# Kernel tuning notes

Measured on AMD Instinct MI355X. Metric: run time of the kernel, lower is better.

The kernel has to match this reference:

```python
import jax, jax.numpy as jnp
from jax import lax
import numpy as np

B, T, I, H, O = 256, 512, 64, 512, 16


def setup_inputs() -> dict:
    key = jax.random.key(0)
    ks = jax.random.split(key, 8)
    s = 1.0 / np.sqrt(H)  # torch RNN/Linear init scale
    return {
        "x": jax.random.normal(ks[0], (B, T, I), dtype=jnp.float32),
        "h0": jnp.zeros((1, B, H), dtype=jnp.float32),
        "W_ih": jax.random.uniform(ks[1], (H, I), jnp.float32, -s, s),
        "W_hh": jax.random.uniform(ks[2], (H, H), jnp.float32, -s, s),
        "b_ih": jax.random.uniform(ks[3], (H,), jnp.float32, -s, s),
        "b_hh": jax.random.uniform(ks[4], (H,), jnp.float32, -s, s),
        "W_fc": jax.random.uniform(ks[5], (O, H), jnp.float32, -s, s),
        "b_fc": jax.random.uniform(ks[6], (O,), jnp.float32, -s, s),
    }


def reference(x, h0, W_ih, W_hh, b_ih, b_hh, W_fc, b_fc):
    # Precompute input projection for all timesteps: (B,T,H)
    xp = jnp.einsum("bti,hi->bth", x, W_ih) + b_ih + b_hh
    W_hh_T = W_hh.T

    def step(h, xt):  # h: (B,H), xt: (B,H)
        h_new = jax.nn.relu(xt + h @ W_hh_T)
        return h_new, None

    h_last, _ = lax.scan(step, h0[0], jnp.swapaxes(xp, 0, 1))  # (B,H)
    out = h_last @ W_fc.T + b_fc  # (B,O)
    # torch module returns (out.unsqueeze(2), hidden) with hidden=(layers,B,H)
    return out[:, :, None], h_last[None, :, :]
```

## Files before the change

kernel.cpp:

```cpp
#include <hip/hip_runtime.h>

#define B_ 256
#define T_ 512
#define I_ 64
#define H_ 512
#define O_ 16

typedef _Float16 half8 __attribute__((ext_vector_type(8)));
typedef _Float16 half4 __attribute__((ext_vector_type(4)));
typedef float    f32x4 __attribute__((ext_vector_type(4)));

#define MFMA16(a, b, c) __builtin_amdgcn_mfma_f32_16x16x32_f16((a), (b), (c), 0, 0, 0)

__device__ inline half8 cvt_h8(f32x4 a, f32x4 b) {
  half8 v;
  v[0] = (_Float16)a[0]; v[1] = (_Float16)a[1]; v[2] = (_Float16)a[2]; v[3] = (_Float16)a[3];
  v[4] = (_Float16)b[0]; v[5] = (_Float16)b[1]; v[6] = (_Float16)b[2]; v[7] = (_Float16)b[3];
  return v;
}

__global__ __launch_bounds__(256, 2)
void xp_prepass(const float* __restrict__ x, const float* __restrict__ W_ih,
                const float* __restrict__ b_ih, const float* __restrict__ b_hh,
                _Float16* __restrict__ xp) {
  const int tid = threadIdx.x, L = tid & 63, w = tid >> 6;
  const int n = L & 15, kq = (L >> 4) & 3;
  const int g = blockIdx.x & 15, tc = blockIdx.x >> 4;

  __shared__ __attribute__((aligned(16))) _Float16 wlih[32 * 2 * 64 * 8];
  __shared__ float biasl[512];
  const half8* wlih8 = (const half8*)wlih;

  #pragma unroll
  for (int u = 0; u < 16; ++u) {
    const int s = tid + u * 256;
    const int jt = s >> 7, c = (s >> 6) & 1, Lp = s & 63;
    const int jl = Lp & 15, kq2 = Lp >> 4;
    const float* p = W_ih + (jt * 16 + jl) * I_ + c * 32 + kq2 * 8;
    ((half8*)wlih)[s] = cvt_h8(*(const f32x4*)(p), *(const f32x4*)(p + 4));
  }
  #pragma unroll
  for (int u = 0; u < 2; ++u) {
    const int idx = tid + u * 256;
    biasl[idx] = b_ih[idx] + b_hh[idx];
  }
  __syncthreads();

  half8 xb[4][2];
  #pragma unroll
  for (int rr = 0; rr < 4; ++rr) {
    const int t = tc * 16 + w * 4 + rr;
    const float* p = x + ((size_t)(g * 16 + n) * T_ + t) * I_ + kq * 8;
    xb[rr][0] = cvt_h8(*(const f32x4*)(p),      *(const f32x4*)(p + 4));
    xb[rr][1] = cvt_h8(*(const f32x4*)(p + 32), *(const f32x4*)(p + 36));
  }

  #pragma unroll 1
  for (int hi = 0; hi < 8; ++hi) {
    half8 o[4][2];
    #pragma unroll
    for (int jt2 = 0; jt2 < 4; ++jt2) {
      const int jt = hi * 4 + jt2;
      const half8 a0 = wlih8[(jt * 2 + 0) * 64 + L];
      const half8 a1 = wlih8[(jt * 2 + 1) * 64 + L];
      const f32x4 bv = *(const f32x4*)&biasl[jt * 16 + 4 * kq];
      #pragma unroll
      for (int rr = 0; rr < 4; ++rr) {
        f32x4 acc; acc[0] = 0.f; acc[1] = 0.f; acc[2] = 0.f; acc[3] = 0.f;
        acc = MFMA16(a0, xb[rr][0], acc);
        acc = MFMA16(a1, xb[rr][1], acc);
        #pragma unroll
        for (int i = 0; i < 4; ++i)
          o[rr][jt2 >> 1][(jt2 & 1) * 4 + i] = (_Float16)(acc[i] + bv[i]);
      }
    }
    #pragma unroll
    for (int rr = 0; rr < 4; ++rr) {
      const int t = tc * 16 + w * 4 + rr;
      _Float16* dst = xp + ((size_t)(t * 16 + g) * 512 + hi * 64 + L) * 16;
      *(half8*)(dst)     = o[rr][0];
      *(half8*)(dst + 8) = o[rr][1];
    }
  }
}

__global__ __launch_bounds__(512, 2)
void rnn_persist(const float* __restrict__ h0, const float* __restrict__ W_hh,
                 const float* __restrict__ W_fc, const float* __restrict__ b_fc,
                 float* __restrict__ out, const _Float16* __restrict__ xp) {
  const int tid = threadIdx.x;
  const int L   = tid & 63;
  const int w   = tid >> 6;
  const int n   = L & 15;
  const int kq  = (L >> 4) & 3;
  const int g   = blockIdx.x;

  __shared__ __attribute__((aligned(16))) _Float16 hb[2 * 16 * 64 * 8];
  __shared__ __attribute__((aligned(16))) _Float16 wlds[8 * 12 * 64 * 8];
  half8* hb8 = (half8*)hb;
  const half8* wl8 = (const half8*)wlds;
  half8* wlw = (half8*)wlds;

  half8 whA[32];
  half8 whV[20];
  #pragma unroll
  for (int ln = 0; ln < 4; ++ln) {
    const int j = w * 64 + ln * 16 + n;
    #pragma unroll
    for (int kc = 0; kc < 8; ++kc) {
      const f32x4* p = (const f32x4*)(W_hh + j * H_ + kc * 32 + kq * 8);
      whA[ln * 8 + kc] = cvt_h8(p[0], p[1]);
    }
    #pragma unroll
    for (int kc = 0; kc < 5; ++kc) {
      const f32x4* p = (const f32x4*)(W_hh + j * H_ + (8 + kc) * 32 + kq * 8);
      whV[ln * 5 + kc] = cvt_h8(p[0], p[1]);
    }
    #pragma unroll
    for (int s = 0; s < 3; ++s) {
      const f32x4* p = (const f32x4*)(W_hh + j * H_ + (13 + s) * 32 + kq * 8);
      wlw[(w * 12 + s * 4 + ln) * 64 + L] = cvt_h8(p[0], p[1]);
    }
  }
  #pragma unroll
  for (int i2 = 0; i2 < 32; ++i2) asm volatile("" : "+a"(whA[i2]));

  #pragma unroll
  for (int u = 0; u < 2; ++u) {
    const int S = tid + u * 512;
    const int k8 = S >> 4, nb = S & 15;
    const float* p = h0 + (g * 16 + nb) * H_ + k8 * 8;
    hb8[S] = cvt_h8(*(const f32x4*)(p), *(const f32x4*)(p + 4));
  }
  __syncthreads();

  half8 xq0, xq1;
  {
    const half8* p0 = (const half8*)(xp + ((size_t)(0 * 16 + g) * 512 + tid) * 16);
    xq0 = p0[0]; xq1 = p0[1];
  }

  #pragma unroll 1
  for (int t = 0; t < T_; ++t) {
    const half8* hbr = hb8 + (t & 1) * 1024;
    half8* hbw = hb8 + ((t + 1) & 1) * 1024;

    f32x4 acc[4];
    #pragma unroll
    for (int ln = 0; ln < 4; ++ln)
      #pragma unroll
      for (int i = 0; i < 4; ++i)
        acc[ln][i] = (float)((ln < 2 ? xq0 : xq1)[(ln & 1) * 4 + i]);

    {
      const int tn = (t + 1) & (T_ - 1);
      const half8* pn = (const half8*)(xp + ((size_t)(tn * 16 + g) * 512 + tid) * 16);
      xq0 = pn[0]; xq1 = pn[1];
    }

    #pragma unroll
    for (int kc = 0; kc < 8; ++kc) {
      const half8 b = hbr[kc * 64 + L];
      #pragma unroll
      for (int ln = 0; ln < 4; ++ln) acc[ln] = MFMA16(whA[ln * 8 + kc], b, acc[ln]);
    }
    #pragma unroll
    for (int kc = 0; kc < 5; ++kc) {
      const half8 b = hbr[(8 + kc) * 64 + L];
      #pragma unroll
      for (int ln = 0; ln < 4; ++ln) acc[ln] = MFMA16(whV[ln * 5 + kc], b, acc[ln]);
    }
    #pragma unroll
    for (int s = 0; s < 3; ++s) {
      const half8 b = hbr[(13 + s) * 64 + L];
      #pragma unroll
      for (int ln = 0; ln < 4; ++ln)
        acc[ln] = MFMA16(wl8[(w * 12 + s * 4 + ln) * 64 + L], b, acc[ln]);
    }

    #pragma unroll
    for (int ln = 0; ln < 4; ++ln) {
      half4 hv;
      #pragma unroll
      for (int i = 0; i < 4; ++i) hv[i] = (_Float16)fmaxf(acc[ln][i], 0.f);
      const int S = (w * 8 + ln * 2 + (kq >> 1)) * 16 + n;
      *(half4*)((_Float16*)hbw + S * 8 + 4 * (kq & 1)) = hv;
    }
    __syncthreads();
  }

  const half8* hf = hb8;
  #pragma unroll
  for (int u = 0; u < 2; ++u) {
    const int ri = tid + u * 512;
    const int k8 = ri >> 4, nb = ri & 15;
    const half8 v = hf[k8 * 16 + nb];
    float* dst = out + 4096 + (g * 16 + nb) * H_ + k8 * 8;
    #pragma unroll
    for (int e = 0; e < 8; ++e) dst[e] = (float)v[e];
  }
  __syncthreads();
  float* wfcf = (float*)wlds;
  #pragma unroll
  for (int u = 0; u < 16; ++u) {
    const int idx = tid + u * 512;
    wfcf[(idx >> 9) * 513 + (idx & 511)] = W_fc[idx];
  }
  __syncthreads();
  if (tid < 256) {
    const int bl = tid >> 4, o = tid & 15;
    float s = 0.f;
    #pragma unroll 8
    for (int k8 = 0; k8 < 64; ++k8) {
      const half8 v = hf[k8 * 16 + bl];
      #pragma unroll
      for (int e = 0; e < 8; ++e) s += (float)v[e] * wfcf[o * 513 + k8 * 8 + e];
    }
    out[(g * 16 + bl) * 16 + o] = s + b_fc[o];
  }
}

extern "C" void kernel_launch(void* const* d_in, const int* in_sizes, int n_in,
                              void* d_out, int out_size, void* d_ws, size_t ws_size,
                              hipStream_t stream) {
  const float* x    = (const float*)d_in[0];
  const float* h0   = (const float*)d_in[1];
  const float* W_ih = (const float*)d_in[2];
  const float* W_hh = (const float*)d_in[3];
  const float* b_ih = (const float*)d_in[4];
  const float* b_hh = (const float*)d_in[5];
  const float* W_fc = (const float*)d_in[6];
  const float* b_fc = (const float*)d_in[7];
  float* out = (float*)d_out;

  _Float16* xp = (_Float16*)d_ws;

  xp_prepass<<<dim3(512), dim3(256), 0, stream>>>(x, W_ih, b_ih, b_hh, xp);
  rnn_persist<<<dim3(16), dim3(512), 0, stream>>>(h0, W_hh, W_fc, b_fc, out, xp);
}
```

Measured before the change: 892.0 us.

## Rotate per-wave K order and prefetch own h chunk before barrier

Each wave now walks the K chunks of the recurrent matmul starting at its own freshly written chunk (2*W), rotating the weight register assignment to match. This lets it read its first B operand right after its own stores and before the barrier, so the first MFMAs of the next step can start with no LDS wait. The per-wave rotation also spreads LDS reads across different addresses. The price is eight template instantiations behind a switch, which increases code size. The final h is still left in buffer 0 because T is even.

```diff
diff --git a/kernel.cpp b/kernel.cpp
--- a/kernel.cpp
+++ b/kernel.cpp
@@ -84,6 +84,104 @@
   }
 }
 
+template <int W>
+__device__ __forceinline__ void rnn_core(const float* __restrict__ W_hh,
+                                         const _Float16* __restrict__ xp,
+                                         half8* hb8, half8* wl8w,
+                                         const int g, const int L) {
+  const int n  = L & 15;
+  const int kq = (L >> 4) & 3;
+  const int tid = W * 64 + L;
+
+  half8 whA[32];
+  half8 whV[20];
+  #pragma unroll
+  for (int ln = 0; ln < 4; ++ln) {
+    const int j = W * 64 + ln * 16 + n;
+    #pragma unroll
+    for (int p = 0; p < 8; ++p) {
+      const int kc = (2 * W + p) & 15;
+      const f32x4* s = (const f32x4*)(W_hh + j * H_ + kc * 32 + kq * 8);
+      whA[ln * 8 + p] = cvt_h8(s[0], s[1]);
+    }
+    #pragma unroll
+    for (int p = 8; p < 13; ++p) {
+      const int kc = (2 * W + p) & 15;
+      const f32x4* s = (const f32x4*)(W_hh + j * H_ + kc * 32 + kq * 8);
+      whV[ln * 5 + (p - 8)] = cvt_h8(s[0], s[1]);
+    }
+    #pragma unroll
+    for (int p = 13; p < 16; ++p) {
+      const int kc = (2 * W + p) & 15;
+      const f32x4* s = (const f32x4*)(W_hh + j * H_ + kc * 32 + kq * 8);
+      wl8w[((p - 13) * 4 + ln) * 64 + L] = cvt_h8(s[0], s[1]);
+    }
+  }
+  #pragma unroll
+  for (int i2 = 0; i2 < 32; ++i2) asm volatile("" : "+a"(whA[i2]));
+
+  half8 xq0, xq1;
+  {
+    const half8* p0 = (const half8*)(xp + ((size_t)(0 * 16 + g) * 512 + tid) * 16);
+    xq0 = p0[0]; xq1 = p0[1];
+  }
+
+  half8* rb = hb8;
+  half8* wb = hb8 + 1024;
+  half8 bq0 = rb[((2 * W) & 15) * 64 + L];
+
+  #pragma unroll 1
+  for (int t = 0; t < T_; ++t) {
+    f32x4 acc[4];
+    #pragma unroll
+    for (int ln = 0; ln < 4; ++ln)
+      #pragma unroll
+      for (int i = 0; i < 4; ++i)
+        acc[ln][i] = (float)((ln < 2 ? xq0 : xq1)[(ln & 1) * 4 + i]);
+
+    {
+      const int tn = (t + 1) & (T_ - 1);
+      const half8* pn = (const half8*)(xp + ((size_t)(tn * 16 + g) * 512 + tid) * 16);
+      xq0 = pn[0]; xq1 = pn[1];
+    }
+
+    #pragma unroll
+    for (int ln = 0; ln < 4; ++ln) acc[ln] = MFMA16(whA[ln * 8 + 0], bq0, acc[ln]);
+    #pragma unroll
+    for (int p = 1; p < 8; ++p) {
+      const half8 b = rb[((2 * W + p) & 15) * 64 + L];
+      #pragma unroll
+      for (int ln = 0; ln < 4; ++ln) acc[ln] = MFMA16(whA[ln * 8 + p], b, acc[ln]);
+    }
+    #pragma unroll
+    for (int p = 8; p < 13; ++p) {
+      const half8 b = rb[((2 * W + p) & 15) * 64 + L];
+      #pragma unroll
+      for (int ln = 0; ln < 4; ++ln) acc[ln] = MFMA16(whV[ln * 5 + (p - 8)], b, acc[ln]);
+    }
+    #pragma unroll
+    for (int p = 13; p < 16; ++p) {
+      const half8 b = rb[((2 * W + p) & 15) * 64 + L];
+      #pragma unroll
+      for (int ln = 0; ln < 4; ++ln)
+        acc[ln] = MFMA16(wl8w[((p - 13) * 4 + ln) * 64 + L], b, acc[ln]);
+    }
+
+    #pragma unroll
+    for (int ln = 0; ln < 4; ++ln) {
+      half4 hv;
+      #pragma unroll
+      for (int i = 0; i < 4; ++i) hv[i] = (_Float16)fmaxf(acc[ln][i], 0.f);
+      const int S = (W * 8 + ln * 2 + (kq >> 1)) * 16 + n;
+      *(half4*)((_Float16*)wb + S * 8 + 4 * (kq & 1)) = hv;
+    }
+    bq0 = wb[((2 * W) & 15) * 64 + L];
+
+    __syncthreads();
+    half8* tmp = rb; rb = wb; wb = tmp;
+  }
+}
+
 __global__ __launch_bounds__(512, 2)
 void rnn_persist(const float* __restrict__ h0, const float* __restrict__ W_hh,
                  const float* __restrict__ W_fc, const float* __restrict__ b_fc,
@@ -91,39 +189,11 @@
   const int tid = threadIdx.x;
   const int L   = tid & 63;
   const int w   = tid >> 6;
-  const int n   = L & 15;
-  const int kq  = (L >> 4) & 3;
   const int g   = blockIdx.x;
 
   __shared__ __attribute__((aligned(16))) _Float16 hb[2 * 16 * 64 * 8];
   __shared__ __attribute__((aligned(16))) _Float16 wlds[8 * 12 * 64 * 8];
   half8* hb8 = (half8*)hb;
-  const half8* wl8 = (const half8*)wlds;
-  half8* wlw = (half8*)wlds;
-
-  half8 whA[32];
-  half8 whV[20];
-  #pragma unroll
-  for (int ln = 0; ln < 4; ++ln) {
-    const int j = w * 64 + ln * 16 + n;
-    #pragma unroll
-    for (int kc = 0; kc < 8; ++kc) {
-      const f32x4* p = (const f32x4*)(W_hh + j * H_ + kc * 32 + kq * 8);
-      whA[ln * 8 + kc] = cvt_h8(p[0], p[1]);
-    }
-    #pragma unroll
-    for (int kc = 0; kc < 5; ++kc) {
-      const f32x4* p = (const f32x4*)(W_hh + j * H_ + (8 + kc) * 32 + kq * 8);
-      whV[ln * 5 + kc] = cvt_h8(p[0], p[1]);
-    }
-    #pragma unroll
-    for (int s = 0; s < 3; ++s) {
-      const f32x4* p = (const f32x4*)(W_hh + j * H_ + (13 + s) * 32 + kq * 8);
-      wlw[(w * 12 + s * 4 + ln) * 64 + L] = cvt_h8(p[0], p[1]);
-    }
-  }
-  #pragma unroll
-  for (int i2 = 0; i2 < 32; ++i2) asm volatile("" : "+a"(whA[i2]));
 
   #pragma unroll
   for (int u = 0; u < 2; ++u) {
@@ -134,59 +204,17 @@
   }
   __syncthreads();
 
-  half8 xq0, xq1;
-  {
-    const half8* p0 = (const half8*)(xp + ((size_t)(0 * 16 + g) * 512 + tid) * 16);
-    xq0 = p0[0]; xq1 = p0[1];
-  }
-
-  #pragma unroll 1
-  for (int t = 0; t < T_; ++t) {
-    const half8* hbr = hb8 + (t & 1) * 1024;
-    half8* hbw = hb8 + ((t + 1) & 1) * 1024;
-
-    f32x4 acc[4];
-    #pragma unroll
-    for (int ln = 0; ln < 4; ++ln)
-      #pragma unroll
-      for (int i = 0; i < 4; ++i)
-        acc[ln][i] = (float)((ln < 2 ? xq0 : xq1)[(ln & 1) * 4 + i]);
-
-    {
-      const int tn = (t + 1) & (T_ - 1);
-      const half8* pn = (const half8*)(xp + ((size_t)(tn * 16 + g) * 512 + tid) * 16);
-      xq0 = pn[0]; xq1 = pn[1];
-    }
-
-    #pragma unroll
-    for (int kc = 0; kc < 8; ++kc) {
-      const half8 b = hbr[kc * 64 + L];
-      #pragma unroll
-      for (int ln = 0; ln < 4; ++ln) acc[ln] = MFMA16(whA[ln * 8 + kc], b, acc[ln]);
-    }
-    #pragma unroll
-    for (int kc = 0; kc < 5; ++kc) {
-      const half8 b = hbr[(8 + kc) * 64 + L];
-      #pragma unroll
-      for (int ln = 0; ln < 4; ++ln) acc[ln] = MFMA16(whV[ln * 5 + kc], b, acc[ln]);
-    }
-    #pragma unroll
-    for (int s = 0; s < 3; ++s) {
-      const half8 b = hbr[(13 + s) * 64 + L];
-      #pragma unroll
-      for (int ln = 0; ln < 4; ++ln)
-        acc[ln] = MFMA16(wl8[(w * 12 + s * 4 + ln) * 64 + L], b, acc[ln]);
-    }
-
-    #pragma unroll
-    for (int ln = 0; ln < 4; ++ln) {
-      half4 hv;
-      #pragma unroll
-      for (int i = 0; i < 4; ++i) hv[i] = (_Float16)fmaxf(acc[ln][i], 0.f);
-      const int S = (w * 8 + ln * 2 + (kq >> 1)) * 16 + n;
-      *(half4*)((_Float16*)hbw + S * 8 + 4 * (kq & 1)) = hv;
-    }
-    __syncthreads();
+  half8* wl8w = (half8*)wlds + (w * 12) * 64;
+
+  switch (w) {
+    case 0: rnn_core<0>(W_hh, xp, hb8, wl8w, g, L); break;
+    case 1: rnn_core<1>(W_hh, xp, hb8, wl8w, g, L); break;
+    case 2: rnn_core<2>(W_hh, xp, hb8, wl8w, g, L); break;
+    case 3: rnn_core<3>(W_hh, xp, hb8, wl8w, g, L); break;
+    case 4: rnn_core<4>(W_hh, xp, hb8, wl8w, g, L); break;
+    case 5: rnn_core<5>(W_hh, xp, hb8, wl8w, g, L); break;
+    case 6: rnn_core<6>(W_hh, xp, hb8, wl8w, g, L); break;
+    default: rnn_core<7>(W_hh, xp, hb8, wl8w, g, L); break;
   }
 
   const half8* hf = hb8;
```

New measurement: 1.063 ms. 19.2% more time.

## Stream last four W_hh k-chunks from global/L2 each step instead of LDS

Applied to the files above, without the earlier changes.

Adds a staging kernel that writes the last four k-chunks of W_hh in fp16 MFMA-fragment layout to workspace. The recurrent kernel reloads these chunks from global memory (expected to be L2-resident) every timestep, double-buffering the loads across MFMA groups. This frees VGPRs, since whV shrinks from 20 to 12 registers, and cuts LDS weight reads to one chunk. The intent is to relieve register pressure and LDS-bandwidth contention in the serial loop, at the cost of per-step global-load latency on the critical path plus an extra kernel launch.

```diff
diff --git a/kernel.cpp b/kernel.cpp
--- a/kernel.cpp
+++ b/kernel.cpp
@@ -17,6 +17,22 @@
   v[0] = (_Float16)a[0]; v[1] = (_Float16)a[1]; v[2] = (_Float16)a[2]; v[3] = (_Float16)a[3];
   v[4] = (_Float16)b[0]; v[5] = (_Float16)b[1]; v[6] = (_Float16)b[2]; v[7] = (_Float16)b[3];
   return v;
+}
+
+__global__ __launch_bounds__(512, 1)
+void wstage(const float* __restrict__ W_hh, _Float16* __restrict__ wbuf) {
+  const int tid = threadIdx.x, L = tid & 63, w = tid >> 6;
+  const int n = L & 15, kq = (L >> 4) & 3;
+  half8* out8 = (half8*)wbuf;
+  #pragma unroll
+  for (int e = 0; e < 4; ++e)
+    #pragma unroll
+    for (int ln = 0; ln < 4; ++ln) {
+      const int j = w * 64 + ln * 16 + n;
+      const int kc = 12 + e;
+      const f32x4* s = (const f32x4*)(W_hh + j * H_ + kc * 32 + kq * 8);
+      out8[(w * 16 + e * 4 + ln) * 64 + L] = cvt_h8(s[0], s[1]);
+    }
 }
 
 __global__ __launch_bounds__(256, 2)
@@ -87,7 +103,8 @@
 __global__ __launch_bounds__(512, 2)
 void rnn_persist(const float* __restrict__ h0, const float* __restrict__ W_hh,
                  const float* __restrict__ W_fc, const float* __restrict__ b_fc,
-                 float* __restrict__ out, const _Float16* __restrict__ xp) {
+                 float* __restrict__ out, const _Float16* __restrict__ xp,
+                 const _Float16* __restrict__ wbuf) {
   const int tid = threadIdx.x;
   const int L   = tid & 63;
   const int w   = tid >> 6;
@@ -96,13 +113,13 @@
   const int g   = blockIdx.x;
 
   __shared__ __attribute__((aligned(16))) _Float16 hb[2 * 16 * 64 * 8];
-  __shared__ __attribute__((aligned(16))) _Float16 wlds[8 * 12 * 64 * 8];
+  __shared__ __attribute__((aligned(16))) char wsmem[16 * 513 * 4];
   half8* hb8 = (half8*)hb;
-  const half8* wl8 = (const half8*)wlds;
-  half8* wlw = (half8*)wlds;
+  half8* wlw = (half8*)wsmem;
+  const half8* wl8 = (const half8*)wsmem;
 
   half8 whA[32];
-  half8 whV[20];
+  half8 whV[12];
   #pragma unroll
   for (int ln = 0; ln < 4; ++ln) {
     const int j = w * 64 + ln * 16 + n;
@@ -112,14 +129,13 @@
       whA[ln * 8 + kc] = cvt_h8(p[0], p[1]);
     }
     #pragma unroll
-    for (int kc = 0; kc < 5; ++kc) {
-      const f32x4* p = (const f32x4*)(W_hh + j * H_ + (8 + kc) * 32 + kq * 8);
-      whV[ln * 5 + kc] = cvt_h8(p[0], p[1]);
-    }
-    #pragma unroll
-    for (int s = 0; s < 3; ++s) {
-      const f32x4* p = (const f32x4*)(W_hh + j * H_ + (13 + s) * 32 + kq * 8);
-      wlw[(w * 12 + s * 4 + ln) * 64 + L] = cvt_h8(p[0], p[1]);
+    for (int kc = 8; kc < 11; ++kc) {
+      const f32x4* p = (const f32x4*)(W_hh + j * H_ + kc * 32 + kq * 8);
+      whV[ln * 3 + (kc - 8)] = cvt_h8(p[0], p[1]);
+    }
+    {
+      const f32x4* p = (const f32x4*)(W_hh + j * H_ + 11 * 32 + kq * 8);
+      wlw[(w * 4 + ln) * 64 + L] = cvt_h8(p[0], p[1]);
     }
   }
   #pragma unroll
@@ -140,11 +156,23 @@
     xq0 = p0[0]; xq1 = p0[1];
   }
 
+  const half8* wsb_base = (const half8*)wbuf + (w * 16) * 64;
+  int zoff = 0;
+
   #pragma unroll 1
   for (int t = 0; t < T_; ++t) {
     const half8* hbr = hb8 + (t & 1) * 1024;
     half8* hbw = hb8 + ((t + 1) & 1) * 1024;
 
+    asm volatile("" : "+v"(zoff));
+    const half8* wsb = wsb_base + zoff;
+
+    half8 ws0[4], ws1[4];
+    #pragma unroll
+    for (int ln = 0; ln < 4; ++ln) ws0[ln] = wsb[(0 * 4 + ln) * 64 + L];
+    #pragma unroll
+    for (int ln = 0; ln < 4; ++ln) ws1[ln] = wsb[(1 * 4 + ln) * 64 + L];
+
     f32x4 acc[4];
     #pragma unroll
     for (int ln = 0; ln < 4; ++ln)
@@ -165,17 +193,40 @@
       for (int ln = 0; ln < 4; ++ln) acc[ln] = MFMA16(whA[ln * 8 + kc], b, acc[ln]);
     }
     #pragma unroll
-    for (int kc = 0; kc < 5; ++kc) {
-      const half8 b = hbr[(8 + kc) * 64 + L];
-      #pragma unroll
-      for (int ln = 0; ln < 4; ++ln) acc[ln] = MFMA16(whV[ln * 5 + kc], b, acc[ln]);
-    }
-    #pragma unroll
-    for (int s = 0; s < 3; ++s) {
-      const half8 b = hbr[(13 + s) * 64 + L];
+    for (int kc = 8; kc < 11; ++kc) {
+      const half8 b = hbr[kc * 64 + L];
+      #pragma unroll
+      for (int ln = 0; ln < 4; ++ln) acc[ln] = MFMA16(whV[ln * 3 + (kc - 8)], b, acc[ln]);
+    }
+    {
+      const half8 b = hbr[11 * 64 + L];
       #pragma unroll
       for (int ln = 0; ln < 4; ++ln)
-        acc[ln] = MFMA16(wl8[(w * 12 + s * 4 + ln) * 64 + L], b, acc[ln]);
+        acc[ln] = MFMA16(wl8[(w * 4 + ln) * 64 + L], b, acc[ln]);
+    }
+    {
+      const half8 b = hbr[12 * 64 + L];
+      #pragma unroll
+      for (int ln = 0; ln < 4; ++ln) acc[ln] = MFMA16(ws0[ln], b, acc[ln]);
+      #pragma unroll
+      for (int ln = 0; ln < 4; ++ln) ws0[ln] = wsb[(2 * 4 + ln) * 64 + L];
+    }
+    {
+      const half8 b = hbr[13 * 64 + L];
+      #pragma unroll
+      for (int ln = 0; ln < 4; ++ln) acc[ln] = MFMA16(ws1[ln], b, acc[ln]);
+      #pragma unroll
+      for (int ln = 0; ln < 4; ++ln) ws1[ln] = wsb[(3 * 4 + ln) * 64 + L];
+    }
+    {
+      const half8 b = hbr[14 * 64 + L];
+      #pragma unroll
+      for (int ln = 0; ln < 4; ++ln) acc[ln] = MFMA16(ws0[ln], b, acc[ln]);
+    }
+    {
+      const half8 b = hbr[15 * 64 + L];
+      #pragma unroll
+      for (int ln = 0; ln < 4; ++ln) acc[ln] = MFMA16(ws1[ln], b, acc[ln]);
     }
 
     #pragma unroll
@@ -200,7 +251,7 @@
     for (int e = 0; e < 8; ++e) dst[e] = (float)v[e];
   }
   __syncthreads();
-  float* wfcf = (float*)wlds;
+  float* wfcf = (float*)wsmem;
   #pragma unroll
   for (int u = 0; u < 16; ++u) {
     const int idx = tid + u * 512;
@@ -233,8 +284,11 @@
   const float* b_fc = (const float*)d_in[7];
   float* out = (float*)d_out;
 
-  _Float16* xp = (_Float16*)d_ws;
-
+  const size_t XP_BYTES = (size_t)B_ * T_ * H_ * 2;
+  _Float16* xp   = (_Float16*)d_ws;
+  _Float16* wbuf = (_Float16*)((char*)d_ws + XP_BYTES);
+
+  wstage<<<dim3(1), dim3(512), 0, stream>>>(W_hh, wbuf);
   xp_prepass<<<dim3(512), dim3(256), 0, stream>>>(x, W_ih, b_ih, b_hh, xp);
-  rnn_persist<<<dim3(16), dim3(512), 0, stream>>>(h0, W_hh, W_fc, b_fc, out, xp);
-}
+  rnn_persist<<<dim3(16), dim3(512), 0, stream>>>(h0, W_hh, W_fc, b_fc, out, xp, wbuf);
+}
```

Result: slower. 1.148 ms (+28.7%).

## Fuse input-projection prepass into persistent RNN kernel with per-chunk flags

Applied to the files above, without the earlier changes.

Merges the input-projection prepass and the persistent recurrence into one launch. Blocks 0-15 run the recurrence, and the remaining 512 blocks compute xp time-chunks and publish completion through per-(chunk,group) release flags. The recurrent blocks spin on acquire loads before consuming each 16-step chunk, so the projection overlaps with the sequential recurrence instead of running before it. This adds a flag memset, spin-wait overhead and a larger 128KB shared allocation. It also relies on the low-indexed recurrent blocks being scheduled alongside the producer blocks to avoid deadlock.

```diff
diff --git a/kernel.cpp b/kernel.cpp
--- a/kernel.cpp
+++ b/kernel.cpp
@@ -19,87 +19,89 @@
   return v;
 }
 
-__global__ __launch_bounds__(256, 2)
-void xp_prepass(const float* __restrict__ x, const float* __restrict__ W_ih,
-                const float* __restrict__ b_ih, const float* __restrict__ b_hh,
-                _Float16* __restrict__ xp) {
-  const int tid = threadIdx.x, L = tid & 63, w = tid >> 6;
-  const int n = L & 15, kq = (L >> 4) & 3;
-  const int g = blockIdx.x & 15, tc = blockIdx.x >> 4;
-
-  __shared__ __attribute__((aligned(16))) _Float16 wlih[32 * 2 * 64 * 8];
-  __shared__ float biasl[512];
-  const half8* wlih8 = (const half8*)wlih;
-
-  #pragma unroll
-  for (int u = 0; u < 16; ++u) {
-    const int s = tid + u * 256;
-    const int jt = s >> 7, c = (s >> 6) & 1, Lp = s & 63;
-    const int jl = Lp & 15, kq2 = Lp >> 4;
-    const float* p = W_ih + (jt * 16 + jl) * I_ + c * 32 + kq2 * 8;
-    ((half8*)wlih)[s] = cvt_h8(*(const f32x4*)(p), *(const f32x4*)(p + 4));
-  }
-  #pragma unroll
-  for (int u = 0; u < 2; ++u) {
-    const int idx = tid + u * 256;
-    biasl[idx] = b_ih[idx] + b_hh[idx];
-  }
-  __syncthreads();
-
-  half8 xb[4][2];
-  #pragma unroll
-  for (int rr = 0; rr < 4; ++rr) {
-    const int t = tc * 16 + w * 4 + rr;
-    const float* p = x + ((size_t)(g * 16 + n) * T_ + t) * I_ + kq * 8;
-    xb[rr][0] = cvt_h8(*(const f32x4*)(p),      *(const f32x4*)(p + 4));
-    xb[rr][1] = cvt_h8(*(const f32x4*)(p + 32), *(const f32x4*)(p + 36));
-  }
-
-  #pragma unroll 1
-  for (int hi = 0; hi < 8; ++hi) {
-    half8 o[4][2];
-    #pragma unroll
-    for (int jt2 = 0; jt2 < 4; ++jt2) {
-      const int jt = hi * 4 + jt2;
-      const half8 a0 = wlih8[(jt * 2 + 0) * 64 + L];
-      const half8 a1 = wlih8[(jt * 2 + 1) * 64 + L];
-      const f32x4 bv = *(const f32x4*)&biasl[jt * 16 + 4 * kq];
-      #pragma unroll
-      for (int rr = 0; rr < 4; ++rr) {
-        f32x4 acc; acc[0] = 0.f; acc[1] = 0.f; acc[2] = 0.f; acc[3] = 0.f;
-        acc = MFMA16(a0, xb[rr][0], acc);
-        acc = MFMA16(a1, xb[rr][1], acc);
-        #pragma unroll
-        for (int i = 0; i < 4; ++i)
-          o[rr][jt2 >> 1][(jt2 & 1) * 4 + i] = (_Float16)(acc[i] + bv[i]);
-      }
-    }
-    #pragma unroll
-    for (int rr = 0; rr < 4; ++rr) {
-      const int t = tc * 16 + w * 4 + rr;
-      _Float16* dst = xp + ((size_t)(t * 16 + g) * 512 + hi * 64 + L) * 16;
-      *(half8*)(dst)     = o[rr][0];
-      *(half8*)(dst + 8) = o[rr][1];
-    }
-  }
-}
-
 __global__ __launch_bounds__(512, 2)
-void rnn_persist(const float* __restrict__ h0, const float* __restrict__ W_hh,
-                 const float* __restrict__ W_fc, const float* __restrict__ b_fc,
-                 float* __restrict__ out, const _Float16* __restrict__ xp) {
+void rnn_fused(const float* __restrict__ x, const float* __restrict__ h0,
+               const float* __restrict__ W_ih, const float* __restrict__ W_hh,
+               const float* __restrict__ b_ih, const float* __restrict__ b_hh,
+               const float* __restrict__ W_fc, const float* __restrict__ b_fc,
+               float* __restrict__ out, _Float16* __restrict__ xp,
+               int* __restrict__ flags) {
   const int tid = threadIdx.x;
   const int L   = tid & 63;
   const int w   = tid >> 6;
   const int n   = L & 15;
   const int kq  = (L >> 4) & 3;
-  const int g   = blockIdx.x;
-
-  __shared__ __attribute__((aligned(16))) _Float16 hb[2 * 16 * 64 * 8];
-  __shared__ __attribute__((aligned(16))) _Float16 wlds[8 * 12 * 64 * 8];
-  half8* hb8 = (half8*)hb;
-  const half8* wl8 = (const half8*)wlds;
-  half8* wlw = (half8*)wlds;
+
+  __shared__ __attribute__((aligned(16))) char smem[131072];
+
+  if (blockIdx.x >= 16) {
+    const int pb = blockIdx.x - 16;
+    const int g = pb & 15, tc = pb >> 4;
+
+    _Float16* wlih = (_Float16*)smem;
+    float* biasl = (float*)(smem + 65536);
+    half8* wlih8w = (half8*)wlih;
+    const half8* wlih8 = (const half8*)wlih;
+
+    #pragma unroll
+    for (int u = 0; u < 8; ++u) {
+      const int s = tid + u * 512;
+      const int jt = s >> 7, c = (s >> 6) & 1, Lp = s & 63;
+      const int jl = Lp & 15, kq2 = Lp >> 4;
+      const float* p = W_ih + (jt * 16 + jl) * I_ + c * 32 + kq2 * 8;
+      wlih8w[s] = cvt_h8(*(const f32x4*)(p), *(const f32x4*)(p + 4));
+    }
+    biasl[tid] = b_ih[tid] + b_hh[tid];
+    __syncthreads();
+
+    half8 xb[2][2];
+    #pragma unroll
+    for (int rr = 0; rr < 2; ++rr) {
+      const int t = tc * 16 + w * 2 + rr;
+      const float* p = x + ((size_t)(g * 16 + n) * T_ + t) * I_ + kq * 8;
+      xb[rr][0] = cvt_h8(*(const f32x4*)(p),      *(const f32x4*)(p + 4));
+      xb[rr][1] = cvt_h8(*(const f32x4*)(p + 32), *(const f32x4*)(p + 36));
+    }
+
+    #pragma unroll 1
+    for (int hi = 0; hi < 8; ++hi) {
+      half8 o[2][2];
+      #pragma unroll
+      for (int jt2 = 0; jt2 < 4; ++jt2) {
+        const int jt = hi * 4 + jt2;
+        const half8 a0 = wlih8[(jt * 2 + 0) * 64 + L];
+        const half8 a1 = wlih8[(jt * 2 + 1) * 64 + L];
+        const f32x4 bv = *(const f32x4*)&biasl[jt * 16 + 4 * kq];
+        #pragma unroll
+        for (int rr = 0; rr < 2; ++rr) {
+          f32x4 acc; acc[0] = 0.f; acc[1] = 0.f; acc[2] = 0.f; acc[3] = 0.f;
+          acc = MFMA16(a0, xb[rr][0], acc);
+          acc = MFMA16(a1, xb[rr][1], acc);
+          #pragma unroll
+          for (int i = 0; i < 4; ++i)
+            o[rr][jt2 >> 1][(jt2 & 1) * 4 + i] = (_Float16)(acc[i] + bv[i]);
+        }
+      }
+      #pragma unroll
+      for (int rr = 0; rr < 2; ++rr) {
+        const int t = tc * 16 + w * 2 + rr;
+        _Float16* dst = xp + ((size_t)(t * 16 + g) * 512 + hi * 64 + L) * 16;
+        *(half8*)(dst)     = o[rr][0];
+        *(half8*)(dst + 8) = o[rr][1];
+      }
+    }
+    __syncthreads();
+    __threadfence();
+    if (tid == 0)
+      __hip_atomic_store(&flags[tc * 16 + g], 1, __ATOMIC_RELEASE,
+                         __HIP_MEMORY_SCOPE_AGENT);
+    return;
+  }
+
+  const int g = blockIdx.x;
+  half8* hb8 = (half8*)smem;
+  half8* wlw = (half8*)(smem + 32768);
+  const half8* wl8 = (const half8*)(smem + 32768);
 
   half8 whA[32];
   half8 whV[20];
@@ -134,6 +136,8 @@
   }
   __syncthreads();
 
+  while (__hip_atomic_load(&flags[g], __ATOMIC_ACQUIRE, __HIP_MEMORY_SCOPE_AGENT) == 0)
+    __builtin_amdgcn_s_sleep(2);
   half8 xq0, xq1;
   {
     const half8* p0 = (const half8*)(xp + ((size_t)(0 * 16 + g) * 512 + tid) * 16);
@@ -154,6 +158,11 @@
 
     {
       const int tn = (t + 1) & (T_ - 1);
+      if ((tn & 15) == 0) {
+        int* fl = &flags[(tn >> 4) * 16 + g];
+        while (__hip_atomic_load(fl, __ATOMIC_ACQUIRE, __HIP_MEMORY_SCOPE_AGENT) == 0)
+          __builtin_amdgcn_s_sleep(2);
+      }
       const half8* pn = (const half8*)(xp + ((size_t)(tn * 16 + g) * 512 + tid) * 16);
       xq0 = pn[0]; xq1 = pn[1];
     }
@@ -200,7 +209,7 @@
     for (int e = 0; e < 8; ++e) dst[e] = (float)v[e];
   }
   __syncthreads();
-  float* wfcf = (float*)wlds;
+  float* wfcf = (float*)(smem + 32768);
   #pragma unroll
   for (int u = 0; u < 16; ++u) {
     const int idx = tid + u * 512;
@@ -233,8 +242,11 @@
   const float* b_fc = (const float*)d_in[7];
   float* out = (float*)d_out;
 
+  const size_t XP_BYTES = (size_t)B_ * T_ * H_ * 2;
   _Float16* xp = (_Float16*)d_ws;
-
-  xp_prepass<<<dim3(512), dim3(256), 0, stream>>>(x, W_ih, b_ih, b_hh, xp);
-  rnn_persist<<<dim3(16), dim3(512), 0, stream>>>(h0, W_hh, W_fc, b_fc, out, xp);
+  int* flags   = (int*)((char*)d_ws + XP_BYTES);
+
+  hipMemsetAsync(flags, 0, 512 * sizeof(int), stream);
+  rnn_fused<<<dim3(16 + 512), dim3(512), 0, stream>>>(x, h0, W_ih, W_hh, b_ih, b_hh,
+                                                      W_fc, b_fc, out, xp, flags);
 }
```

New measurement: 1.551 ms. +73.9%, slower.
